# Optimization experiments

Measured on AMD Instinct MI355X. Metric: run time of the kernel, lower is better.

Reference implementation:

```python
import jax, jax.numpy as jnp
import numpy as np

B, K, NP = 2, 48, 25            # batch, context_length, grid_x*grid_y
C, H, L = 768, 12, 6            # n_embd, n_head, n_layer
COLORS, VOCAB, IS = 10, 40, 26  # color_num, vocab_size, intention_size
MAXT = 1000                     # max_timestep
TOK = NP + 4                    # tokens per timestep (rtg, 25 states, action, pnp, intention)
T = K * TOK                     # total sequence length


def layernorm(x, g, b, eps=1e-5):
    m = x.mean(-1, keepdims=True)
    v = ((x - m) ** 2).mean(-1, keepdims=True)
    return (x - m) * jax.lax.rsqrt(v + eps) * g + b


def causal_attn(x, wq, bq, wk, bk, wv, bv, wo, bo):
    Bx, Tx, Cx = x.shape
    hd = Cx // H
    def heads(w, bb):
        return (x @ w + bb).reshape(Bx, Tx, H, hd).transpose(0, 2, 1, 3)
    q, k, v = heads(wq, bq), heads(wk, bk), heads(wv, bv)
    att = jnp.einsum('bhqd,bhkd->bhqk', q, k) * (1.0 / np.sqrt(hd))
    mask = jnp.tril(jnp.ones((Tx, Tx), bool))
    att = jnp.where(mask, att, -jnp.inf)
    att = jax.nn.softmax(att, axis=-1)
    y = jnp.einsum('bhqk,bhkd->bhqd', att, v).transpose(0, 2, 1, 3).reshape(Bx, Tx, Cx)
    return y @ wo + bo


def setup_inputs() -> dict:
    key = jax.random.key(0)
    ks = iter(jax.random.split(key, 64))
    def nrm(shape):
        return jax.random.normal(next(ks), shape, jnp.float32) * 0.02
    inp = dict(
        states=jax.random.randint(next(ks), (B, K * NP), 0, COLORS),
        actions=jax.random.randint(next(ks), (B, K), 0, VOCAB),
        rtgs=jax.random.normal(next(ks), (B, K), jnp.float32),
        timesteps=jax.random.randint(next(ks), (B, K), 0, MAXT + 1),
        pnp=jax.random.normal(next(ks), (B, K, NP), jnp.float32),
        intentions=jax.random.randint(next(ks), (B, K, 2), 0, IS),
        pos_emb=nrm((K + 1, C)),               # (block_size, C)
        global_pos_emb=nrm((MAXT + 1, C)),
        state_tab=nrm((COLORS, C)),
        action_tab=nrm((VOCAB, C)),
        ret_W=nrm((1, C)), ret_b=jnp.zeros((C,)),
        pnp_W=nrm((NP, C)), pnp_b=jnp.zeros((C,)),
        src_tab=nrm((IS, C)), dst_tab=nrm((IS, C)),
        int_W=nrm((2 * C, C)), int_b=jnp.zeros((C,)),
        ln1_g=jnp.ones((L, C)), ln1_b=jnp.zeros((L, C)),
        ln2_g=jnp.ones((L, C)), ln2_b=jnp.zeros((L, C)),
        Wq=nrm((L, C, C)), bq=jnp.zeros((L, C)),
        Wk=nrm((L, C, C)), bk=jnp.zeros((L, C)),
        Wv=nrm((L, C, C)), bv=jnp.zeros((L, C)),
        Wo=nrm((L, C, C)), bo=jnp.zeros((L, C)),
        Wm1=nrm((L, C, 4 * C)), bm1=jnp.zeros((L, 4 * C)),
        Wm2=nrm((L, 4 * C, C)), bm2=jnp.zeros((L, C)),
        lnf_g=jnp.ones((C,)), lnf_b=jnp.zeros((C,)),
        Whs=nrm((C, COLORS)), bhs=jnp.zeros((COLORS,)),
        Wha=nrm((C, VOCAB)), bha=jnp.zeros((VOCAB,)),
        Whr=nrm((C, 1)), bhr=jnp.zeros((1,)),
        Whi=nrm((C, 2 * IS)), bhi=jnp.zeros((2 * IS,)),
    )
    return inp


def reference(states, actions, rtgs, timesteps, pnp, intentions,
              pos_emb, global_pos_emb, state_tab, action_tab,
              ret_W, ret_b, pnp_W, pnp_b, src_tab, dst_tab, int_W, int_b,
              ln1_g, ln1_b, ln2_g, ln2_b, Wq, bq, Wk, bk, Wv, bv, Wo, bo,
              Wm1, bm1, Wm2, bm2, lnf_g, lnf_b,
              Whs, bhs, Wha, bha, Whr, bhr, Whi, bhi):
    # --- embeddings, interleaved as [rtg, state_0..24, action, pnp, intention] per timestep ---
    st = state_tab[states].reshape(B, K, NP, C)                    # strided writes 1+i::TOK
    ae = action_tab[actions][:, :, None, :]
    re = (rtgs[..., None] @ ret_W + ret_b)[:, :, None, :]          # rtgs.unsqueeze(-1) -> Linear(1,C)
    pe = (pnp @ pnp_W + pnp_b)[:, :, None, :]
    ie_in = jnp.concatenate([src_tab[intentions[..., 0]], dst_tab[intentions[..., 1]]], axis=-1)
    ie = (ie_in @ int_W + int_b)[:, :, None, :]
    tok = jnp.concatenate([re, st, ae, pe, ie], axis=2).reshape(B, T, C)
    # --- positions: gather global + local pos_emb[:block_size-1], repeat_interleave by TOK ---
    pos = global_pos_emb[timesteps] + pos_emb[:K][None]            # (B, K, C)
    x = tok + jnp.repeat(pos, TOK, axis=1)
    # --- transformer stack (dropout p=0) ---
    def blk(h, p):
        l1g, l1b, l2g, l2b, wq, bq_, wk, bk_, wv, bv_, wo, bo_, w1, b1, w2, b2 = p
        h = h + causal_attn(layernorm(h, l1g, l1b), wq, bq_, wk, bk_, wv, bv_, wo, bo_)
        m = layernorm(h, l2g, l2b)
        h = h + jax.nn.gelu(m @ w1 + b1, approximate=False) @ w2 + b2
        return h, None
    x, _ = jax.lax.scan(blk, x, (ln1_g, ln1_b, ln2_g, ln2_b, Wq, bq, Wk, bk, Wv, bv, Wo, bo, Wm1, bm1, Wm2, bm2))
    x = layernorm(x, lnf_g, lnf_b)
    xr = x.reshape(B, K, TOK, C)
    logits = x @ Whs + bhs                                         # (B, T, COLORS)
    logit_action = xr[:, :, NP + 1] @ Wha + bha                    # (B, K, VOCAB)
    logit_rtg = (xr[:, :, 0] @ Whr + bhr)[..., 0]                  # (B, K)
    li = xr[:, :, NP + 3] @ Whi + bhi                              # (B, K, 2*IS)
    return logits, logit_action, logit_rtg, li[..., :IS], li[..., IS:]
```

## Files before the change

### kernel.cpp

```cpp
#include <hip/hip_runtime.h>
#include <hip/hip_bf16.h>
#include <math.h>


typedef __hip_bfloat16 bf16;
typedef __attribute__((ext_vector_type(4))) short s4v;
typedef __attribute__((ext_vector_type(8))) short s8v;
typedef __attribute__((ext_vector_type(4))) float f4v;
typedef unsigned int u32;

#define DEV static __device__ __forceinline__

constexpr int NBATCH = 2;
constexpr int NK   = 48;
constexpr int NNP  = 25;
constexpr int NC   = 768;
constexpr int NH   = 12;
constexpr int NL   = 6;
constexpr int NTOK = 29;
constexpr int NT   = NK * NTOK;
constexpr int NM   = NBATCH * NT;
constexpr int MPAD = 2816;

DEV float bs2f(short s) {
  unsigned u = ((unsigned)(unsigned short)s) << 16;
  float f; __builtin_memcpy(&f, &u, 4); return f;
}
DEV short f2bs(float f) {
  bf16 h = __float2bfloat16(f);
  short s; __builtin_memcpy(&s, &h, 2); return s;
}

DEV void async16(const short* g, short* l) {
  __builtin_amdgcn_global_load_lds(
      (const __attribute__((address_space(1))) u32*)g,
      (__attribute__((address_space(3))) u32*)l, 16, 0, 0);
}

__global__ __launch_bounds__(256) void transpose_kernel(
    const float* __restrict__ src, bf16* __restrict__ dst, int R, int C)
{
  int c0 = blockIdx.x * 32, r0 = blockIdx.y * 32;
  __shared__ float tl[32][33];
  int rr = threadIdx.x >> 5, cc = threadIdx.x & 31;
#pragma unroll
  for (int p = 0; p < 4; p++)
    tl[rr + p * 8][cc] = src[(long)(r0 + rr + p * 8) * C + c0 + cc];
  __syncthreads();
#pragma unroll
  for (int p = 0; p < 4; p++)
    dst[(long)(c0 + rr + p * 8) * R + r0 + cc] = __float2bfloat16(tl[cc][rr + p * 8]);
}

__global__ __launch_bounds__(256) void transpose_layer_kernel(
    const float* __restrict__ Wq, const float* __restrict__ Wk,
    const float* __restrict__ Wv, const float* __restrict__ Wo,
    const float* __restrict__ Wm1, const float* __restrict__ Wm2,
    bf16* __restrict__ WqkvT, bf16* __restrict__ WoT,
    bf16* __restrict__ Wm1T, bf16* __restrict__ Wm2T, int multi)
{
  int blk = blockIdx.x;
  int l = blk / 1728, t = blk - l * 1728;
  long so = (long)l * 768 * 768;
  long mo = (long)l * 768 * 3072;
  long dl = multi ? l : 0;
  const float* src; bf16* dst; int R, C, tile;
  if (t < 432) {
    int m = t / 144; tile = t - m * 144;
    src = (m == 0 ? Wq : (m == 1 ? Wk : Wv)) + so;
    dst = WqkvT + dl * (2304L * 768) + (long)m * 768 * 768; R = 768; C = 768;
  } else if (t < 576)  { src = Wo + so;  dst = WoT  + dl * (768L * 768);  tile = t - 432;  R = 768;  C = 768;  }
  else if (t < 1152)   { src = Wm1 + mo; dst = Wm1T + dl * (3072L * 768); tile = t - 576;  R = 768;  C = 3072; }
  else                 { src = Wm2 + mo; dst = Wm2T + dl * (768L * 3072); tile = t - 1152; R = 3072; C = 768;  }
  int ct = C / 64;
  int tr = tile / ct, tc = tile - tr * ct;
  int r0 = tr * 64, c0 = tc * 64;

  __shared__ short tl[64][66];
  int t4 = threadIdx.x & 15, rr = threadIdx.x >> 4;
#pragma unroll
  for (int p = 0; p < 4; p++) {
    int row = rr + p * 16;
    f4v v = *(const f4v*)(src + (long)(r0 + row) * C + c0 + t4 * 4);
    tl[t4 * 4 + 0][row] = f2bs(v.x);
    tl[t4 * 4 + 1][row] = f2bs(v.y);
    tl[t4 * 4 + 2][row] = f2bs(v.z);
    tl[t4 * 4 + 3][row] = f2bs(v.w);
  }
  __syncthreads();
#pragma unroll
  for (int p = 0; p < 4; p++) {
    int drow = rr + p * 16;
    s4v w = *(const s4v*)&tl[drow][t4 * 4];
    *(s4v*)((short*)dst + (long)(c0 + drow) * R + r0 + t4 * 4) = w;
  }
}

__global__ __launch_bounds__(256) void gather_ie_kernel(
    const int* __restrict__ intentions, const float* __restrict__ src_tab,
    const float* __restrict__ dst_tab, bf16* __restrict__ ie_in)
{
  int idx = blockIdx.x * 256 + threadIdx.x;
  if (idx >= 96 * 1536) return;
  int row = idx / 1536, col = idx - row * 1536;
  float v;
  if (col < 768) v = src_tab[intentions[row * 2 + 0] * 768 + col];
  else           v = dst_tab[intentions[row * 2 + 1] * 768 + col - 768];
  ie_in[idx] = __float2bfloat16(v);
}

__global__ __launch_bounds__(256) void embed_kernel(
    const int* __restrict__ states, const int* __restrict__ actions,
    const float* __restrict__ rtgs, const int* __restrict__ timesteps,
    const float* __restrict__ pnp,
    const float* __restrict__ pos_emb, const float* __restrict__ gpe,
    const float* __restrict__ state_tab, const float* __restrict__ action_tab,
    const float* __restrict__ retW, const float* __restrict__ retb,
    const float* __restrict__ pnpW, const float* __restrict__ pnpb,
    const bf16* __restrict__ ieb, float* __restrict__ X)
{
  int bk = blockIdx.x;
  int b = bk / NK, ts = bk - b * NK;
  int c = blockIdx.y * 256 + threadIdx.x;

  float rtg = rtgs[bk];
  int tstep = timesteps[bk];
  int act   = actions[bk];

  long base = (long)(b * NT + ts * NTOK) * NC;
  float pos = gpe[(long)tstep * NC + c] + pos_emb[ts * NC + c];

  X[base + c] = rtg * retW[c] + retb[c] + pos;
  const int* sp = states + bk * NNP;
#pragma unroll
  for (int i = 0; i < NNP; i++)
    X[base + (1 + i) * NC + c] = state_tab[sp[i] * NC + c] + pos;
  X[base + 26 * NC + c] = action_tab[act * NC + c] + pos;
  float ap = pnpb[c];
  const float* pv = pnp + bk * NNP;
#pragma unroll
  for (int i = 0; i < NNP; i++) ap += pv[i] * pnpW[i * NC + c];
  X[base + 27 * NC + c] = ap + pos;
  X[base + 28 * NC + c] = __bfloat162float(ieb[bk * NC + c]) + pos;
}

__global__ __launch_bounds__(256) void ln_kernel(
    const float* __restrict__ X, bf16* __restrict__ XN,
    const float* __restrict__ g, const float* __restrict__ bt)
{
  int row = blockIdx.x, tid = threadIdx.x;
  const float* x = X + (long)row * NC;
  float v0 = x[tid], v1 = x[tid + 256], v2 = x[tid + 512];
  float s = v0 + v1 + v2;
#pragma unroll
  for (int o = 32; o > 0; o >>= 1) s += __shfl_down(s, o, 64);
  __shared__ float red[8];
  if ((tid & 63) == 0) red[tid >> 6] = s;
  __syncthreads();
  float mean = (red[0] + red[1] + red[2] + red[3]) * (1.0f / NC);
  float d0 = v0 - mean, d1 = v1 - mean, d2 = v2 - mean;
  float qq = d0 * d0 + d1 * d1 + d2 * d2;
#pragma unroll
  for (int o = 32; o > 0; o >>= 1) qq += __shfl_down(qq, o, 64);
  __syncthreads();
  if ((tid & 63) == 0) red[tid >> 6] = qq;
  __syncthreads();
  float var = (red[0] + red[1] + red[2] + red[3]) * (1.0f / NC);
  float rs = 1.0f / sqrtf(var + 1e-5f);
  bf16* xn = XN + (long)row * NC;
  xn[tid      ] = __float2bfloat16(d0 * rs * g[tid      ] + bt[tid      ]);
  xn[tid + 256] = __float2bfloat16(d1 * rs * g[tid + 256] + bt[tid + 256]);
  xn[tid + 512] = __float2bfloat16(d2 * rs * g[tid + 512] + bt[tid + 512]);
}

template<int BM, int BN>
__global__ __launch_bounds__(256) void gemm_kernel(
    const bf16* __restrict__ A, const bf16* __restrict__ WT,
    const float* __restrict__ b0, const float* __restrict__ b1,
    const float* __restrict__ b2, int Nsplit,
    bf16* __restrict__ outb, float* __restrict__ resid,
    int M, int N, int K, int flags)
{
  constexpr int IM  = BM / 64;
  constexpr int JN  = BN / 16;
  constexpr int ACH = BM / 64;
  constexpr int BCH = BN / 64;
  __shared__ __align__(1024) short As[2][BM * 32];
  __shared__ __align__(1024) short Bs[2][BN * 32];

  int tid = threadIdx.x, wave = tid >> 6, lane = tid & 63;
  int quad = lane >> 4, l16 = lane & 15;
  int m0 = blockIdx.y * BM, n0 = blockIdx.x * BN;
  int wm = wave * (BM / 4);
  int lr = lane >> 2, lc = (lane & 3) * 8;

  const short* Ag = (const short*)A + (long)m0 * K + lc;
  const short* Bg = (const short*)WT + (long)n0 * K + lc;

  const short* ag[ACH]; int alo[ACH];
#pragma unroll
  for (int c = 0; c < ACH; c++) {
    int rbase = wave * (16 * ACH) + c * 16;
    ag[c] = Ag + (long)(rbase + lr) * K;
    alo[c] = rbase * 32;
  }
  const short* bg[BCH]; int blo[BCH];
#pragma unroll
  for (int c = 0; c < BCH; c++) {
    int rbase = wave * (16 * BCH) + c * 16;
    bg[c] = Bg + (long)(rbase + lr) * K;
    blo[c] = rbase * 32;
  }

  f4v zero4 = {0.f, 0.f, 0.f, 0.f};
  f4v acc[IM][JN];
#pragma unroll
  for (int i = 0; i < IM; i++)
#pragma unroll
    for (int j = 0; j < JN; j++) acc[i][j] = zero4;

  int nk = K >> 5;
#pragma unroll
  for (int c = 0; c < ACH; c++) async16(ag[c], &As[0][alo[c]]);
#pragma unroll
  for (int c = 0; c < BCH; c++) async16(bg[c], &Bs[0][blo[c]]);
  __syncthreads();

  for (int kt = 0; kt < nk; kt++) {
    int cur = kt & 1, nxt = cur ^ 1;
    if (kt + 1 < nk) {
      int ko = (kt + 1) << 5;
#pragma unroll
      for (int c = 0; c < ACH; c++) async16(ag[c] + ko, &As[nxt][alo[c]]);
#pragma unroll
      for (int c = 0; c < BCH; c++) async16(bg[c] + ko, &Bs[nxt][blo[c]]);
    }
    s8v af[IM], bf8[JN];
#pragma unroll
    for (int i = 0; i < IM; i++) {
      const short* p = &As[cur][(wm + i * 16 + l16) * 32 + quad * 8];
      af[i].lo = *(const s4v*)p; af[i].hi = *(const s4v*)(p + 4);
    }
#pragma unroll
    for (int j = 0; j < JN; j++) {
      const short* p = &Bs[cur][(j * 16 + l16) * 32 + quad * 8];
      bf8[j].lo = *(const s4v*)p; bf8[j].hi = *(const s4v*)(p + 4);
    }
#pragma unroll
    for (int i = 0; i < IM; i++)
#pragma unroll
      for (int j = 0; j < JN; j++)
        acc[i][j] = __builtin_amdgcn_mfma_f32_16x16x32_bf16(af[i], bf8[j], acc[i][j], 0, 0, 0);
    __syncthreads();
  }

#pragma unroll
  for (int i = 0; i < IM; i++) {
    int rbase = m0 + wm + i * 16 + quad * 4;
#pragma unroll
    for (int j = 0; j < JN; j++) {
      int bc = n0 + j * 16;
      int wsel = bc / Nsplit;
      const float* bp = wsel == 0 ? b0 : (wsel == 1 ? b1 : b2);
      float bv = bp[bc - wsel * Nsplit + l16];
      int col = bc + l16;
#pragma unroll
      for (int r = 0; r < 4; r++) {
        int row = rbase + r;
        if (row < M) {
          float v = acc[i][j][r] + bv;
          if (flags & 1) v = 0.5f * v * (1.0f + erff(v * 0.70710678118654752f));
          if (flags & 2) resid[(long)row * N + col] += v;
          else outb[(long)row * N + col] = __float2bfloat16(v);
        }
      }
    }
  }
}

constexpr int ASTR = 72;

__global__ __launch_bounds__(256) void attn_kernel(
    const bf16* __restrict__ QKV, bf16* __restrict__ Yg)
{
  int qt = blockIdx.x, h = blockIdx.y, b = blockIdx.z;
  int q0 = qt * 64;
  int tid = threadIdx.x, wave = tid >> 6, lane = tid & 63, quad = lane >> 4, l16 = lane & 15;

  __shared__ short Qs[64 * ASTR];
  __shared__ short Ks[64 * ASTR];
  __shared__ short Vt[64 * ASTR];
  __shared__ short Ps[64 * ASTR];

  int r = tid >> 2, c16 = (tid & 3) * 16;
  const short* src = (const short*)QKV;
  s8v zz = {0,0,0,0,0,0,0,0};

  s8v qv0 = zz, qv1 = zz;
  if (q0 + r < NT) {
    const s8v* p = (const s8v*)(src + (long)(b * NT + q0 + r) * 2304 + h * 64 + c16);
    qv0 = p[0]; qv1 = p[1];
  }
  {
    short* qp = &Qs[r * ASTR + c16];
    *(s4v*)(qp    ) = qv0.lo; *(s4v*)(qp + 4) = qv0.hi;
    *(s4v*)(qp + 8) = qv1.lo; *(s4v*)(qp + 12) = qv1.hi;
  }

  f4v zero4 = {0.f, 0.f, 0.f, 0.f};
  f4v Of[4];
#pragma unroll
  for (int j = 0; j < 4; j++) Of[j] = zero4;
  float m_r[4], l_r[4];
#pragma unroll
  for (int rg = 0; rg < 4; rg++) { m_r[rg] = -1e30f; l_r[rg] = 0.f; }

  int kend = q0 + 63; if (kend > NT - 1) kend = NT - 1;

  s8v kv0 = zz, kv1 = zz, vv0 = zz, vv1 = zz;
  if (r < NT) {
    const s8v* pk = (const s8v*)(src + (long)(b * NT + r) * 2304 + 768 + h * 64 + c16);
    kv0 = pk[0]; kv1 = pk[1];
    const s8v* pvv = (const s8v*)(src + (long)(b * NT + r) * 2304 + 1536 + h * 64 + c16);
    vv0 = pvv[0]; vv1 = pvv[1];
  }

  for (int k0 = 0; k0 <= kend; k0 += 64) {
    __syncthreads();
    {
      short* kp = &Ks[r * ASTR + c16];
      *(s4v*)(kp    ) = kv0.lo; *(s4v*)(kp + 4) = kv0.hi;
      *(s4v*)(kp + 8) = kv1.lo; *(s4v*)(kp + 12) = kv1.hi;
      short* vt = &Vt[c16 * ASTR + r];
      vt[ 0 * ASTR] = vv0.s0; vt[ 1 * ASTR] = vv0.s1; vt[ 2 * ASTR] = vv0.s2; vt[ 3 * ASTR] = vv0.s3;
      vt[ 4 * ASTR] = vv0.s4; vt[ 5 * ASTR] = vv0.s5; vt[ 6 * ASTR] = vv0.s6; vt[ 7 * ASTR] = vv0.s7;
      vt[ 8 * ASTR] = vv1.s0; vt[ 9 * ASTR] = vv1.s1; vt[10 * ASTR] = vv1.s2; vt[11 * ASTR] = vv1.s3;
      vt[12 * ASTR] = vv1.s4; vt[13 * ASTR] = vv1.s5; vt[14 * ASTR] = vv1.s6; vt[15 * ASTR] = vv1.s7;
    }
    __syncthreads();

    int k1 = k0 + 64;
    s8v nk0 = zz, nk1 = zz, nv0 = zz, nv1 = zz;
    if (k1 <= kend && k1 + r < NT) {
      const s8v* pk = (const s8v*)(src + (long)(b * NT + k1 + r) * 2304 + 768 + h * 64 + c16);
      nk0 = pk[0]; nk1 = pk[1];
      const s8v* pvv = (const s8v*)(src + (long)(b * NT + k1 + r) * 2304 + 1536 + h * 64 + c16);
      nv0 = pvv[0]; nv1 = pvv[1];
    }

    f4v sa[4];
#pragma unroll
    for (int j = 0; j < 4; j++) sa[j] = zero4;
#pragma unroll
    for (int ks = 0; ks < 2; ks++) {
      const short* pa = &Qs[(wave * 16 + l16) * ASTR + ks * 32 + quad * 8];
      s8v aq; aq.lo = *(const s4v*)pa; aq.hi = *(const s4v*)(pa + 4);
#pragma unroll
      for (int j = 0; j < 4; j++) {
        const short* pb = &Ks[(j * 16 + l16) * ASTR + ks * 32 + quad * 8];
        s8v bk8; bk8.lo = *(const s4v*)pb; bk8.hi = *(const s4v*)(pb + 4);
        sa[j] = __builtin_amdgcn_mfma_f32_16x16x32_bf16(aq, bk8, sa[j], 0, 0, 0);
      }
    }

#pragma unroll
    for (int j = 0; j < 4; j++) {
#pragma unroll
      for (int rg = 0; rg < 4; rg++) {
        int gq = q0 + wave * 16 + quad * 4 + rg;
        int gk = k0 + j * 16 + l16;
        sa[j][rg] = (gk <= gq && gq < NT) ? sa[j][rg] * 0.125f : -1e30f;
      }
    }

#pragma unroll
    for (int rg = 0; rg < 4; rg++) {
      float mx = fmaxf(fmaxf(sa[0][rg], sa[1][rg]), fmaxf(sa[2][rg], sa[3][rg]));
      mx = fmaxf(mx, __shfl_xor(mx, 1));
      mx = fmaxf(mx, __shfl_xor(mx, 2));
      mx = fmaxf(mx, __shfl_xor(mx, 4));
      mx = fmaxf(mx, __shfl_xor(mx, 8));
      float mn = fmaxf(m_r[rg], mx);
      float al = __expf(m_r[rg] - mn);
      m_r[rg] = mn;
      float ps = 0.f;
#pragma unroll
      for (int j = 0; j < 4; j++) {
        float e = __expf(sa[j][rg] - mn);
        sa[j][rg] = e;
        ps += e;
      }
      ps += __shfl_xor(ps, 1);
      ps += __shfl_xor(ps, 2);
      ps += __shfl_xor(ps, 4);
      ps += __shfl_xor(ps, 8);
      l_r[rg] = l_r[rg] * al + ps;
#pragma unroll
      for (int j = 0; j < 4; j++) Of[j][rg] *= al;
    }

#pragma unroll
    for (int j = 0; j < 4; j++)
#pragma unroll
      for (int rg = 0; rg < 4; rg++)
        Ps[(wave * 16 + quad * 4 + rg) * ASTR + j * 16 + l16] = f2bs(sa[j][rg]);
    __syncthreads();

#pragma unroll
    for (int ks = 0; ks < 2; ks++) {
      const short* pa = &Ps[(wave * 16 + l16) * ASTR + ks * 32 + quad * 8];
      s8v ap8; ap8.lo = *(const s4v*)pa; ap8.hi = *(const s4v*)(pa + 4);
#pragma unroll
      for (int j = 0; j < 4; j++) {
        const short* pb = &Vt[(j * 16 + l16) * ASTR + ks * 32 + quad * 8];
        s8v vp8; vp8.lo = *(const s4v*)pb; vp8.hi = *(const s4v*)(pb + 4);
        Of[j] = __builtin_amdgcn_mfma_f32_16x16x32_bf16(ap8, vp8, Of[j], 0, 0, 0);
      }
    }

    kv0 = nk0; kv1 = nk1; vv0 = nv0; vv1 = nv1;
  }

#pragma unroll
  for (int rg = 0; rg < 4; rg++) {
    int rloc = wave * 16 + quad * 4 + rg;
    int gq = q0 + rloc;
    if (gq < NT) {
      float inv = 1.0f / l_r[rg];
#pragma unroll
      for (int j = 0; j < 4; j++) {
        float ov = Of[j][rg] * inv;
        Yg[(long)(b * NT + gq) * NC + h * 64 + j * 16 + l16] = __float2bfloat16(ov);
      }
    }
  }
}

__global__ __launch_bounds__(256) void head_logits_kernel(
    const bf16* __restrict__ XN, const float* __restrict__ Whs,
    const float* __restrict__ bhs, float* __restrict__ out)
{
  int idx = blockIdx.x * 256 + threadIdx.x;
  if (idx >= NM * 10) return;
  int row = idx / 10, n = idx - row * 10;
  const short* x = (const short*)XN + (long)row * NC;
  float a0 = bhs[n], a1 = 0.f, a2 = 0.f, a3 = 0.f;
  for (int k = 0; k < NC; k += 4) {
    a0 += bs2f(x[k    ]) * Whs[(k    ) * 10 + n];
    a1 += bs2f(x[k + 1]) * Whs[(k + 1) * 10 + n];
    a2 += bs2f(x[k + 2]) * Whs[(k + 2) * 10 + n];
    a3 += bs2f(x[k + 3]) * Whs[(k + 3) * 10 + n];
  }
  out[idx] = a0 + a1 + a2 + a3;
}

__global__ __launch_bounds__(128) void head_small_kernel(
    const bf16* __restrict__ XN,
    const float* __restrict__ Wha, const float* __restrict__ bha,
    const float* __restrict__ Whr, const float* __restrict__ bhr,
    const float* __restrict__ Whi, const float* __restrict__ bhi,
    float* __restrict__ outA, float* __restrict__ outR,
    float* __restrict__ outS, float* __restrict__ outD)
{
  int blk = blockIdx.x;
  int b = blk / NK, ts = blk - b * NK;
  int tid = threadIdx.x;
  if (tid >= 93) return;
  const short* xs = (const short*)XN;
  if (tid < 40) {
    long row = (long)(b * NT + ts * NTOK + 26) * NC;
    float a0 = bha[tid], a1 = 0.f, a2 = 0.f, a3 = 0.f;
    for (int k = 0; k < NC; k += 4) {
      a0 += bs2f(xs[row + k    ]) * Wha[(k    ) * 40 + tid];
      a1 += bs2f(xs[row + k + 1]) * Wha[(k + 1) * 40 + tid];
      a2 += bs2f(xs[row + k + 2]) * Wha[(k + 2) * 40 + tid];
      a3 += bs2f(xs[row + k + 3]) * Wha[(k + 3) * 40 + tid];
    }
    outA[blk * 40 + tid] = a0 + a1 + a2 + a3;
  } else if (tid == 40) {
    long row = (long)(b * NT + ts * NTOK) * NC;
    float a0 = bhr[0], a1 = 0.f, a2 = 0.f, a3 = 0.f;
    for (int k = 0; k < NC; k += 4) {
      a0 += bs2f(xs[row + k    ]) * Whr[k    ];
      a1 += bs2f(xs[row + k + 1]) * Whr[k + 1];
      a2 += bs2f(xs[row + k + 2]) * Whr[k + 2];
      a3 += bs2f(xs[row + k + 3]) * Whr[k + 3];
    }
    outR[blk] = a0 + a1 + a2 + a3;
  } else {
    int n = tid - 41;
    long row = (long)(b * NT + ts * NTOK + 28) * NC;
    float a0 = bhi[n], a1 = 0.f, a2 = 0.f, a3 = 0.f;
    for (int k = 0; k < NC; k += 4) {
      a0 += bs2f(xs[row + k    ]) * Whi[(k    ) * 52 + n];
      a1 += bs2f(xs[row + k + 1]) * Whi[(k + 1) * 52 + n];
      a2 += bs2f(xs[row + k + 2]) * Whi[(k + 2) * 52 + n];
      a3 += bs2f(xs[row + k + 3]) * Whi[(k + 3) * 52 + n];
    }
    if (n < 26) outS[blk * 26 + n] = a0 + a1 + a2 + a3;
    else        outD[blk * 26 + (n - 26)] = a0 + a1 + a2 + a3;
  }
}

extern "C" void kernel_launch(void* const* d_in, const int* in_sizes, int n_in,
                              void* d_out, int out_size, void* d_ws, size_t ws_size,
                              hipStream_t stream)
{
  (void)in_sizes; (void)n_in; (void)out_size;

  const int*   states     = (const int*)  d_in[0];
  const int*   actions    = (const int*)  d_in[1];
  const float* rtgs       = (const float*)d_in[2];
  const int*   timesteps  = (const int*)  d_in[3];
  const float* pnp        = (const float*)d_in[4];
  const int*   intentions = (const int*)  d_in[5];
  const float* pos_emb    = (const float*)d_in[6];
  const float* gpe        = (const float*)d_in[7];
  const float* state_tab  = (const float*)d_in[8];
  const float* action_tab = (const float*)d_in[9];
  const float* retW  = (const float*)d_in[10];
  const float* retb  = (const float*)d_in[11];
  const float* pnpW  = (const float*)d_in[12];
  const float* pnpb  = (const float*)d_in[13];
  const float* src_tab = (const float*)d_in[14];
  const float* dst_tab = (const float*)d_in[15];
  const float* intW  = (const float*)d_in[16];
  const float* intb  = (const float*)d_in[17];
  const float* ln1g  = (const float*)d_in[18];
  const float* ln1b  = (const float*)d_in[19];
  const float* ln2g  = (const float*)d_in[20];
  const float* ln2b  = (const float*)d_in[21];
  const float* Wq = (const float*)d_in[22];
  const float* bq = (const float*)d_in[23];
  const float* Wk = (const float*)d_in[24];
  const float* bk = (const float*)d_in[25];
  const float* Wv = (const float*)d_in[26];
  const float* bv = (const float*)d_in[27];
  const float* Wo = (const float*)d_in[28];
  const float* bo = (const float*)d_in[29];
  const float* Wm1 = (const float*)d_in[30];
  const float* bm1 = (const float*)d_in[31];
  const float* Wm2 = (const float*)d_in[32];
  const float* bm2 = (const float*)d_in[33];
  const float* lnfg = (const float*)d_in[34];
  const float* lnfb = (const float*)d_in[35];
  const float* Whs = (const float*)d_in[36];
  const float* bhs = (const float*)d_in[37];
  const float* Wha = (const float*)d_in[38];
  const float* bha = (const float*)d_in[39];
  const float* Whr = (const float*)d_in[40];
  const float* bhr = (const float*)d_in[41];
  const float* Whi = (const float*)d_in[42];
  const float* bhi = (const float*)d_in[43];

  char* wsb = (char*)d_ws;
  float* X   = (float*)(wsb);
  bf16* XN   = (bf16*)(wsb + 8650752);
  bf16* QKVb = (bf16*)(wsb + 12976128);
  bf16* Yb   = (bf16*)(wsb + 25952256);
  bf16* H1   = QKVb;
  bf16* WTbase = (bf16*)(wsb + 30277632);

  const size_t NEED_BIG = 30277632UL + 84934656UL + 2949120UL;
  bool big = ws_size >= NEED_BIG;

  long sQKV = 2304L * 768, sO = 768L * 768, sM1 = 3072L * 768, sM2 = 768L * 3072;
  bf16 *WqkvT, *WoT, *Wm1T, *Wm2T, *intWT;
  if (big) {
    WqkvT = WTbase;
    WoT   = WqkvT + 6 * sQKV;
    Wm1T  = WoT   + 6 * sO;
    Wm2T  = Wm1T  + 6 * sM1;
    intWT = Wm2T  + 6 * sM2;
  } else {
    WqkvT = WTbase;
    WoT   = WqkvT + sQKV;
    Wm1T  = WoT + sO;
    Wm2T  = Wm1T + sM1;
    intWT = WTbase;
  }
  bf16* ie_in = intWT + 768L * 1536;
  bf16* ieb   = ie_in + 128L * 1536;

  float* out0 = (float*)d_out;
  float* out1 = out0 + 27840;
  float* out2 = out1 + 3840;
  float* out3 = out2 + 96;
  float* out4 = out3 + 2496;

  transpose_kernel<<<dim3(24, 48), 256, 0, stream>>>(intW, intWT, 1536, 768);
  gather_ie_kernel<<<(96 * 1536 + 255) / 256, 256, 0, stream>>>(intentions, src_tab, dst_tab, ie_in);
  gemm_kernel<64, 64><<<dim3(12, 2), 256, 0, stream>>>(ie_in, intWT, intb, intb, intb, 768,
      ieb, nullptr, 96, 768, 1536, 0);
  embed_kernel<<<dim3(96, 3), 256, 0, stream>>>(
      states, actions, rtgs, timesteps, pnp, pos_emb, gpe, state_tab, action_tab,
      retW, retb, pnpW, pnpb, ieb, X);

  if (big)
    transpose_layer_kernel<<<1728 * NL, 256, 0, stream>>>(
        Wq, Wk, Wv, Wo, Wm1, Wm2, WqkvT, WoT, Wm1T, Wm2T, 1);

  for (int l = 0; l < NL; l++) {
    const long wofs = (long)l * NC * NC;
    const long mofs = (long)l * NC * 4 * NC;
    if (!big)
      transpose_layer_kernel<<<1728, 256, 0, stream>>>(
          Wq + wofs, Wk + wofs, Wv + wofs, Wo + wofs, Wm1 + mofs, Wm2 + mofs,
          WqkvT, WoT, Wm1T, Wm2T, 0);
    bf16* wqkv = big ? WqkvT + l * sQKV : WqkvT;
    bf16* wo   = big ? WoT   + l * sO   : WoT;
    bf16* wm1  = big ? Wm1T  + l * sM1  : Wm1T;
    bf16* wm2  = big ? Wm2T  + l * sM2  : Wm2T;

    ln_kernel<<<NM, 256, 0, stream>>>(X, XN, ln1g + l * NC, ln1b + l * NC);
    gemm_kernel<128, 64><<<dim3(36, 22), 256, 0, stream>>>(XN, wqkv,
        bq + l * NC, bk + l * NC, bv + l * NC, 768, QKVb, nullptr, NM, 2304, NC, 0);
    attn_kernel<<<dim3(22, NH, NBATCH), 256, 0, stream>>>(QKVb, Yb);
    gemm_kernel<64, 64><<<dim3(12, 44), 256, 0, stream>>>(Yb, wo,
        bo + l * NC, bo + l * NC, bo + l * NC, 768, nullptr, X, NM, 768, NC, 2);
    ln_kernel<<<NM, 256, 0, stream>>>(X, XN, ln2g + l * NC, ln2b + l * NC);
    gemm_kernel<128, 64><<<dim3(48, 22), 256, 0, stream>>>(XN, wm1,
        bm1 + l * 4 * NC, bm1 + l * 4 * NC, bm1 + l * 4 * NC, 4 * NC, H1, nullptr,
        NM, 3072, NC, 1);
    gemm_kernel<64, 64><<<dim3(12, 44), 256, 0, stream>>>(H1, wm2,
        bm2 + l * NC, bm2 + l * NC, bm2 + l * NC, 768, nullptr, X, NM, 768, 4 * NC, 2);
  }
  ln_kernel<<<NM, 256, 0, stream>>>(X, XN, lnfg, lnfb);
  head_logits_kernel<<<(NM * 10 + 255) / 256, 256, 0, stream>>>(XN, Whs, bhs, out0);
  head_small_kernel<<<NBATCH * NK, 128, 0, stream>>>(XN, Wha, bha, Whr, bhr, Whi, bhi,
      out1, out2, out3, out4);
}
```

Before: 1.624 ms.

## Vectorize layernorm per-wave, widen weight transpose tiles, merge head kernels

LayerNorm now handles one row per wave, using float4 loads and bf16x4 stores and xor-shuffle reductions with no shared memory or block barriers, and launches a quarter as many blocks. The weight transpose kernel processes 128x64 tiles, writing 16-byte bf16 vectors instead of 8-byte ones, which halves the block count. The two output-head kernels are merged into a single launch, saving one launch. The transpose reads LDS column-wise with a 66-short stride, which may cause bank conflicts.

```diff
diff --git a/kernel.cpp b/kernel.cpp
--- a/kernel.cpp
+++ b/kernel.cpp
@@ -60,39 +60,42 @@
     bf16* __restrict__ Wm1T, bf16* __restrict__ Wm2T, int multi)
 {
   int blk = blockIdx.x;
-  int l = blk / 1728, t = blk - l * 1728;
+  int l = blk / 864, t = blk - l * 864;
   long so = (long)l * 768 * 768;
   long mo = (long)l * 768 * 3072;
   long dl = multi ? l : 0;
   const float* src; bf16* dst; int R, C, tile;
-  if (t < 432) {
-    int m = t / 144; tile = t - m * 144;
+  if (t < 216) {
+    int m = t / 72; tile = t - m * 72;
     src = (m == 0 ? Wq : (m == 1 ? Wk : Wv)) + so;
     dst = WqkvT + dl * (2304L * 768) + (long)m * 768 * 768; R = 768; C = 768;
-  } else if (t < 576)  { src = Wo + so;  dst = WoT  + dl * (768L * 768);  tile = t - 432;  R = 768;  C = 768;  }
-  else if (t < 1152)   { src = Wm1 + mo; dst = Wm1T + dl * (3072L * 768); tile = t - 576;  R = 768;  C = 3072; }
-  else                 { src = Wm2 + mo; dst = Wm2T + dl * (768L * 3072); tile = t - 1152; R = 3072; C = 768;  }
+  } else if (t < 288)  { src = Wo + so;  dst = WoT  + dl * (768L * 768);  tile = t - 216; R = 768;  C = 768;  }
+  else if (t < 576)    { src = Wm1 + mo; dst = Wm1T + dl * (3072L * 768); tile = t - 288; R = 768;  C = 3072; }
+  else                 { src = Wm2 + mo; dst = Wm2T + dl * (768L * 3072); tile = t - 576; R = 3072; C = 768;  }
   int ct = C / 64;
   int tr = tile / ct, tc = tile - tr * ct;
-  int r0 = tr * 64, c0 = tc * 64;
-
-  __shared__ short tl[64][66];
-  int t4 = threadIdx.x & 15, rr = threadIdx.x >> 4;
+  int r0 = tr * 128, c0 = tc * 64;
+
+  __shared__ short tl[128][66];
+  int cg = threadIdx.x & 15, rg = threadIdx.x >> 4;
+#pragma unroll
+  for (int p = 0; p < 8; p++) {
+    int row = rg + p * 16;
+    f4v v = *(const f4v*)(src + (long)(r0 + row) * C + c0 + cg * 4);
+    tl[row][cg * 4 + 0] = f2bs(v.x);
+    tl[row][cg * 4 + 1] = f2bs(v.y);
+    tl[row][cg * 4 + 2] = f2bs(v.z);
+    tl[row][cg * 4 + 3] = f2bs(v.w);
+  }
+  __syncthreads();
 #pragma unroll
   for (int p = 0; p < 4; p++) {
-    int row = rr + p * 16;
-    f4v v = *(const f4v*)(src + (long)(r0 + row) * C + c0 + t4 * 4);
-    tl[t4 * 4 + 0][row] = f2bs(v.x);
-    tl[t4 * 4 + 1][row] = f2bs(v.y);
-    tl[t4 * 4 + 2][row] = f2bs(v.z);
-    tl[t4 * 4 + 3][row] = f2bs(v.w);
-  }
-  __syncthreads();
-#pragma unroll
-  for (int p = 0; p < 4; p++) {
-    int drow = rr + p * 16;
-    s4v w = *(const s4v*)&tl[drow][t4 * 4];
-    *(s4v*)((short*)dst + (long)(c0 + drow) * R + r0 + t4 * 4) = w;
+    int d = rg + p * 16;
+    const short* base = &tl[cg * 8][d];
+    s8v w;
+    w.s0 = base[0 * 66]; w.s1 = base[1 * 66]; w.s2 = base[2 * 66]; w.s3 = base[3 * 66];
+    w.s4 = base[4 * 66]; w.s5 = base[5 * 66]; w.s6 = base[6 * 66]; w.s7 = base[7 * 66];
+    *(s8v*)((short*)dst + (long)(c0 + d) * R + r0 + cg * 8) = w;
   }
 }
 
@@ -148,29 +151,45 @@
     const float* __restrict__ X, bf16* __restrict__ XN,
     const float* __restrict__ g, const float* __restrict__ bt)
 {
-  int row = blockIdx.x, tid = threadIdx.x;
+  int row = blockIdx.x * 4 + (threadIdx.x >> 6);
+  int lane = threadIdx.x & 63;
   const float* x = X + (long)row * NC;
-  float v0 = x[tid], v1 = x[tid + 256], v2 = x[tid + 512];
-  float s = v0 + v1 + v2;
-#pragma unroll
-  for (int o = 32; o > 0; o >>= 1) s += __shfl_down(s, o, 64);
-  __shared__ float red[8];
-  if ((tid & 63) == 0) red[tid >> 6] = s;
-  __syncthreads();
-  float mean = (red[0] + red[1] + red[2] + red[3]) * (1.0f / NC);
-  float d0 = v0 - mean, d1 = v1 - mean, d2 = v2 - mean;
-  float qq = d0 * d0 + d1 * d1 + d2 * d2;
-#pragma unroll
-  for (int o = 32; o > 0; o >>= 1) qq += __shfl_down(qq, o, 64);
-  __syncthreads();
-  if ((tid & 63) == 0) red[tid >> 6] = qq;
-  __syncthreads();
-  float var = (red[0] + red[1] + red[2] + red[3]) * (1.0f / NC);
+  f4v v0 = *(const f4v*)(x + lane * 4);
+  f4v v1 = *(const f4v*)(x + 256 + lane * 4);
+  f4v v2 = *(const f4v*)(x + 512 + lane * 4);
+  float s = v0.x + v0.y + v0.z + v0.w + v1.x + v1.y + v1.z + v1.w
+          + v2.x + v2.y + v2.z + v2.w;
+#pragma unroll
+  for (int o = 32; o > 0; o >>= 1) s += __shfl_xor(s, o);
+  float mean = s * (1.0f / NC);
+  f4v d0, d1, d2;
+  d0.x = v0.x - mean; d0.y = v0.y - mean; d0.z = v0.z - mean; d0.w = v0.w - mean;
+  d1.x = v1.x - mean; d1.y = v1.y - mean; d1.z = v1.z - mean; d1.w = v1.w - mean;
+  d2.x = v2.x - mean; d2.y = v2.y - mean; d2.z = v2.z - mean; d2.w = v2.w - mean;
+  float qq = d0.x*d0.x + d0.y*d0.y + d0.z*d0.z + d0.w*d0.w
+           + d1.x*d1.x + d1.y*d1.y + d1.z*d1.z + d1.w*d1.w
+           + d2.x*d2.x + d2.y*d2.y + d2.z*d2.z + d2.w*d2.w;
+#pragma unroll
+  for (int o = 32; o > 0; o >>= 1) qq += __shfl_xor(qq, o);
+  float var = qq * (1.0f / NC);
   float rs = 1.0f / sqrtf(var + 1e-5f);
-  bf16* xn = XN + (long)row * NC;
-  xn[tid      ] = __float2bfloat16(d0 * rs * g[tid      ] + bt[tid      ]);
-  xn[tid + 256] = __float2bfloat16(d1 * rs * g[tid + 256] + bt[tid + 256]);
-  xn[tid + 512] = __float2bfloat16(d2 * rs * g[tid + 512] + bt[tid + 512]);
+  short* xn = (short*)XN + (long)row * NC;
+  f4v g0 = *(const f4v*)(g + lane * 4);
+  f4v g1 = *(const f4v*)(g + 256 + lane * 4);
+  f4v g2 = *(const f4v*)(g + 512 + lane * 4);
+  f4v b0 = *(const f4v*)(bt + lane * 4);
+  f4v b1 = *(const f4v*)(bt + 256 + lane * 4);
+  f4v b2 = *(const f4v*)(bt + 512 + lane * 4);
+  s4v w0, w1, w2;
+  w0.x = f2bs(d0.x * rs * g0.x + b0.x); w0.y = f2bs(d0.y * rs * g0.y + b0.y);
+  w0.z = f2bs(d0.z * rs * g0.z + b0.z); w0.w = f2bs(d0.w * rs * g0.w + b0.w);
+  w1.x = f2bs(d1.x * rs * g1.x + b1.x); w1.y = f2bs(d1.y * rs * g1.y + b1.y);
+  w1.z = f2bs(d1.z * rs * g1.z + b1.z); w1.w = f2bs(d1.w * rs * g1.w + b1.w);
+  w2.x = f2bs(d2.x * rs * g2.x + b2.x); w2.y = f2bs(d2.y * rs * g2.y + b2.y);
+  w2.z = f2bs(d2.z * rs * g2.z + b2.z); w2.w = f2bs(d2.w * rs * g2.w + b2.w);
+  *(s4v*)(xn + lane * 4)       = w0;
+  *(s4v*)(xn + 256 + lane * 4) = w1;
+  *(s4v*)(xn + 512 + lane * 4) = w2;
 }
 
 template<int BM, int BN>
@@ -436,37 +455,36 @@
   }
 }
 
-__global__ __launch_bounds__(256) void head_logits_kernel(
+__global__ __launch_bounds__(256) void head_kernel(
     const bf16* __restrict__ XN, const float* __restrict__ Whs,
-    const float* __restrict__ bhs, float* __restrict__ out)
-{
-  int idx = blockIdx.x * 256 + threadIdx.x;
-  if (idx >= NM * 10) return;
-  int row = idx / 10, n = idx - row * 10;
-  const short* x = (const short*)XN + (long)row * NC;
-  float a0 = bhs[n], a1 = 0.f, a2 = 0.f, a3 = 0.f;
-  for (int k = 0; k < NC; k += 4) {
-    a0 += bs2f(x[k    ]) * Whs[(k    ) * 10 + n];
-    a1 += bs2f(x[k + 1]) * Whs[(k + 1) * 10 + n];
-    a2 += bs2f(x[k + 2]) * Whs[(k + 2) * 10 + n];
-    a3 += bs2f(x[k + 3]) * Whs[(k + 3) * 10 + n];
-  }
-  out[idx] = a0 + a1 + a2 + a3;
-}
-
-__global__ __launch_bounds__(128) void head_small_kernel(
-    const bf16* __restrict__ XN,
+    const float* __restrict__ bhs,
     const float* __restrict__ Wha, const float* __restrict__ bha,
     const float* __restrict__ Whr, const float* __restrict__ bhr,
     const float* __restrict__ Whi, const float* __restrict__ bhi,
-    float* __restrict__ outA, float* __restrict__ outR,
-    float* __restrict__ outS, float* __restrict__ outD)
-{
-  int blk = blockIdx.x;
+    float* __restrict__ out0, float* __restrict__ outA,
+    float* __restrict__ outR, float* __restrict__ outS,
+    float* __restrict__ outD)
+{
+  int tid = threadIdx.x;
+  const short* xs = (const short*)XN;
+  if (blockIdx.x < 109) {
+    int idx = blockIdx.x * 256 + tid;
+    if (idx >= NM * 10) return;
+    int row = idx / 10, n = idx - row * 10;
+    const short* x = xs + (long)row * NC;
+    float a0 = bhs[n], a1 = 0.f, a2 = 0.f, a3 = 0.f;
+    for (int k = 0; k < NC; k += 4) {
+      a0 += bs2f(x[k    ]) * Whs[(k    ) * 10 + n];
+      a1 += bs2f(x[k + 1]) * Whs[(k + 1) * 10 + n];
+      a2 += bs2f(x[k + 2]) * Whs[(k + 2) * 10 + n];
+      a3 += bs2f(x[k + 3]) * Whs[(k + 3) * 10 + n];
+    }
+    out0[idx] = a0 + a1 + a2 + a3;
+    return;
+  }
+  int blk = blockIdx.x - 109;
   int b = blk / NK, ts = blk - b * NK;
-  int tid = threadIdx.x;
   if (tid >= 93) return;
-  const short* xs = (const short*)XN;
   if (tid < 40) {
     long row = (long)(b * NT + ts * NTOK + 26) * NC;
     float a0 = bha[tid], a1 = 0.f, a2 = 0.f, a3 = 0.f;
@@ -597,14 +615,14 @@
       retW, retb, pnpW, pnpb, ieb, X);
 
   if (big)
-    transpose_layer_kernel<<<1728 * NL, 256, 0, stream>>>(
+    transpose_layer_kernel<<<864 * NL, 256, 0, stream>>>(
         Wq, Wk, Wv, Wo, Wm1, Wm2, WqkvT, WoT, Wm1T, Wm2T, 1);
 
   for (int l = 0; l < NL; l++) {
     const long wofs = (long)l * NC * NC;
     const long mofs = (long)l * NC * 4 * NC;
     if (!big)
-      transpose_layer_kernel<<<1728, 256, 0, stream>>>(
+      transpose_layer_kernel<<<864, 256, 0, stream>>>(
           Wq + wofs, Wk + wofs, Wv + wofs, Wo + wofs, Wm1 + mofs, Wm2 + mofs,
           WqkvT, WoT, Wm1T, Wm2T, 0);
     bf16* wqkv = big ? WqkvT + l * sQKV : WqkvT;
@@ -612,21 +630,20 @@
     bf16* wm1  = big ? Wm1T  + l * sM1  : Wm1T;
     bf16* wm2  = big ? Wm2T  + l * sM2  : Wm2T;
 
-    ln_kernel<<<NM, 256, 0, stream>>>(X, XN, ln1g + l * NC, ln1b + l * NC);
+    ln_kernel<<<NM / 4, 256, 0, stream>>>(X, XN, ln1g + l * NC, ln1b + l * NC);
     gemm_kernel<128, 64><<<dim3(36, 22), 256, 0, stream>>>(XN, wqkv,
         bq + l * NC, bk + l * NC, bv + l * NC, 768, QKVb, nullptr, NM, 2304, NC, 0);
     attn_kernel<<<dim3(22, NH, NBATCH), 256, 0, stream>>>(QKVb, Yb);
     gemm_kernel<64, 64><<<dim3(12, 44), 256, 0, stream>>>(Yb, wo,
         bo + l * NC, bo + l * NC, bo + l * NC, 768, nullptr, X, NM, 768, NC, 2);
-    ln_kernel<<<NM, 256, 0, stream>>>(X, XN, ln2g + l * NC, ln2b + l * NC);
+    ln_kernel<<<NM / 4, 256, 0, stream>>>(X, XN, ln2g + l * NC, ln2b + l * NC);
     gemm_kernel<128, 64><<<dim3(48, 22), 256, 0, stream>>>(XN, wm1,
         bm1 + l * 4 * NC, bm1 + l * 4 * NC, bm1 + l * 4 * NC, 4 * NC, H1, nullptr,
         NM, 3072, NC, 1);
     gemm_kernel<64, 64><<<dim3(12, 44), 256, 0, stream>>>(H1, wm2,
         bm2 + l * NC, bm2 + l * NC, bm2 + l * NC, 768, nullptr, X, NM, 768, 4 * NC, 2);
   }
-  ln_kernel<<<NM, 256, 0, stream>>>(X, XN, lnfg, lnfb);
-  head_logits_kernel<<<(NM * 10 + 255) / 256, 256, 0, stream>>>(XN, Whs, bhs, out0);
-  head_small_kernel<<<NBATCH * NK, 128, 0, stream>>>(XN, Wha, bha, Whr, bhr, Whi, bhi,
-      out1, out2, out3, out4);
-}
+  ln_kernel<<<NM / 4, 256, 0, stream>>>(X, XN, lnfg, lnfb);
+  head_kernel<<<109 + NBATCH * NK, 256, 0, stream>>>(XN, Whs, bhs, Wha, bha,
+      Whr, bhr, Whi, bhi, out0, out1, out2, out3, out4);
+}
```

Result: faster. 1.589 ms (-2.1%).
